# Kernel optimization log

Hardware: AMD Instinct MI355X
Metric: run time of the kernel (lower is better)

Reference implementation:

```python
import jax, jax.numpy as jnp
import numpy as np

N = 50000     # nodes
E = 600000    # directed edges (avg degree 12)
F_IN = 128    # num_features
H = 128       # hidden_units
C = 16        # num_classes
G = 500       # graphs in batch


def setup_inputs() -> dict:
    key = jax.random.key(0)
    ks = jax.random.split(key, 6)
    x = jax.random.normal(ks[0], (N, F_IN), jnp.float32)
    edge_src = jax.random.randint(ks[1], (E,), 0, N, jnp.int32)
    edge_dst = jax.random.randint(ks[2], (E,), 0, N, jnp.int32)
    batch = jnp.sort(jax.random.randint(ks[3], (N,), 0, G, jnp.int32))
    W1 = jax.random.normal(ks[4], (F_IN, H), jnp.float32) / np.float32(np.sqrt(F_IN))
    b1 = jnp.zeros((H,), jnp.float32)
    W2 = jax.random.normal(ks[5], (H, C), jnp.float32) / np.float32(np.sqrt(H))
    b2 = jnp.zeros((C,), jnp.float32)
    return {"x": x, "W1": W1, "b1": b1, "W2": W2, "b2": b2,
            "edge_src": edge_src, "edge_dst": edge_dst, "batch": batch}


def _gcn_conv(x, W, b, src, dst, norm):
    # linear transform then normalized scatter-add aggregation (PyG GCNConv)
    h = x @ W                                   # [N, out]
    msg = h[src] * norm[:, None]                # [E+N, out]
    return jax.ops.segment_sum(msg, dst, num_segments=N) + b


def reference(x, W1, b1, W2, b2, edge_src, edge_dst, batch):
    # add self-loops
    loops = jnp.arange(N, dtype=edge_src.dtype)
    src = jnp.concatenate([edge_src, loops])
    dst = jnp.concatenate([edge_dst, loops])
    # symmetric normalization D^-1/2 A D^-1/2 (in-degree at targets)
    deg = jax.ops.segment_sum(jnp.ones_like(dst, jnp.float32), dst, num_segments=N)
    dis = jax.lax.rsqrt(deg)  # deg >= 1 because of self-loops
    norm = dis[src] * dis[dst]

    h = jax.nn.relu(_gcn_conv(x, W1, b1, src, dst, norm))
    h = _gcn_conv(h, W2, b2, src, dst, norm)

    # scatter_mean pooling over graphs
    counts = jax.ops.segment_sum(jnp.ones((N,), jnp.float32), batch, num_segments=G)
    pooled = jax.ops.segment_sum(h, batch, num_segments=G) / jnp.maximum(counts, 1.0)[:, None]
    return jax.nn.log_softmax(pooled, axis=1)
```

## Files before the change

kernel.cpp:

```cpp
#include <hip/hip_runtime.h>
#include <hip/hip_bf16.h>


#define NN 50000
#define EE 600000
#define FIN 128
#define HH 128
#define CC 16
#define GG 500
#define ETOT (EE + NN)
#define SBLK 196

typedef unsigned short ushort_t;
typedef unsigned int uint_t;

typedef __attribute__((ext_vector_type(8))) short bf16x8;
typedef __attribute__((ext_vector_type(8))) ushort_t u16x8;
typedef __attribute__((ext_vector_type(4))) ushort_t u16x4;
typedef __attribute__((ext_vector_type(4))) float f32x4;
typedef __attribute__((ext_vector_type(2))) float f32x2;

__device__ inline ushort_t f2bf(float f) {
    uint_t u = __float_as_uint(f);
    u = (u + 0x7FFFu + ((u >> 16) & 1u)) >> 16;
    return (ushort_t)u;
}
__device__ inline float bf2f(ushort_t b) {
    return __uint_as_float(((uint_t)b) << 16);
}

__global__ void init_kernel(int* cnt, float* pooled) {
    int i = blockIdx.x * blockDim.x + threadIdx.x;
    if (i < NN) cnt[i] = 0;
    if (i < GG * CC) pooled[i] = 0.0f;
}

__global__ void count_kernel(const int* __restrict__ edge_dst,
                             int* __restrict__ cnt, int* __restrict__ seq) {
    int idx = blockIdx.x * blockDim.x + threadIdx.x;
    if (idx < EE) seq[idx] = atomicAdd(&cnt[edge_dst[idx]], 1);
}

__device__ inline int block_excl_scan(int v, int t, int* total) {
    __shared__ int wsum[4];
    int lane = t & 63, wv = t >> 6;
    int inc = v;
    for (int off = 1; off < 64; off <<= 1) {
        int n = __shfl_up(inc, off);
        if (lane >= off) inc += n;
    }
    if (lane == 63) wsum[wv] = inc;
    __syncthreads();
    int off_w = 0;
    for (int w = 0; w < wv; w++) off_w += wsum[w];
    *total = wsum[0] + wsum[1] + wsum[2] + wsum[3];
    return off_w + inc - v;
}

__global__ __launch_bounds__(256) void scanA_kernel(const int* __restrict__ cnt,
                                                    int* __restrict__ rowptr,
                                                    float* __restrict__ dis,
                                                    int* __restrict__ bsum) {
    int t = threadIdx.x;
    int i = blockIdx.x * 256 + t;
    int d = 0;
    if (i < NN) {
        d = cnt[i] + 1;
        dis[i] = rsqrtf((float)d);
    }
    int total;
    int excl = block_excl_scan(d, t, &total);
    if (i < NN) rowptr[i] = excl;
    if (t == 0) bsum[blockIdx.x] = total;
}

__global__ __launch_bounds__(256) void scanBC_kernel(int* __restrict__ rowptr,
                                                     const int* __restrict__ bsum) {
    __shared__ int sb[256];
    int t = threadIdx.x;
    int v = (t < SBLK) ? bsum[t] : 0;
    int total;
    int ex = block_excl_scan(v, t, &total);
    sb[t] = ex;
    __syncthreads();
    int myoff = sb[blockIdx.x];
    int i = blockIdx.x * 256 + t;
    if (i < NN) rowptr[i] += myoff;
    if (blockIdx.x == 0 && t == 0) rowptr[NN] = ETOT;
}

__global__ void fill_kernel(const int* __restrict__ edge_src,
                            const int* __restrict__ edge_dst,
                            const int* __restrict__ rowptr,
                            const int* __restrict__ seq,
                            int* __restrict__ csr) {
    int idx = blockIdx.x * blockDim.x + threadIdx.x;
    if (idx < EE) {
        int d = edge_dst[idx];
        csr[rowptr[d] + seq[idx]] = edge_src[idx];
    } else if (idx < ETOT) {
        int n = idx - EE;
        csr[rowptr[n + 1] - 1] = n;
    }
}

__global__ __launch_bounds__(256) void gemm1_kernel(const float* __restrict__ x,
                                                    const float* __restrict__ W1,
                                                    const float* __restrict__ dis,
                                                    unsigned char* __restrict__ hb8) {
    __shared__ ushort_t xs[64 * 136];
    __shared__ ushort_t wt[128 * 136];
    int t = threadIdx.x;
    int row0 = blockIdx.x * 64;
    for (int i = 0; i < 8; i++) {
        int slot = t + i * 256;
        int r = slot >> 5, k4 = slot & 31;
        int gr = row0 + r;
        float4 v = (gr < NN) ? ((const float4*)x)[gr * 32 + k4]
                             : make_float4(0.f, 0.f, 0.f, 0.f);
        u16x4 bv = { f2bf(v.x), f2bf(v.y), f2bf(v.z), f2bf(v.w) };
        *(u16x4*)(&xs[r * 136 + k4 * 4]) = bv;
    }
    for (int i = 0; i < 16; i++) {
        int slot = t + i * 256;
        int k = slot >> 5, c4 = slot & 31;
        float4 v = ((const float4*)W1)[k * 32 + c4];
        wt[(c4 * 4 + 0) * 136 + k] = f2bf(v.x);
        wt[(c4 * 4 + 1) * 136 + k] = f2bf(v.y);
        wt[(c4 * 4 + 2) * 136 + k] = f2bf(v.z);
        wt[(c4 * 4 + 3) * 136 + k] = f2bf(v.w);
    }
    __syncthreads();

    int wave = t >> 6, lane = t & 63;
    int m = lane & 15, quad = lane >> 4;
    f32x4 acc[8];
    for (int ct = 0; ct < 8; ct++) acc[ct] = (f32x4)(0.0f);

    for (int ko = 0; ko < 4; ko++) {
        bf16x8 a = *(const bf16x8*)(&xs[(16 * wave + m) * 136 + ko * 32 + quad * 8]);
        for (int ct = 0; ct < 8; ct++) {
            bf16x8 b = *(const bf16x8*)(&wt[(ct * 16 + m) * 136 + ko * 32 + quad * 8]);
            acc[ct] = __builtin_amdgcn_mfma_f32_16x16x32_bf16(a, b, acc[ct], 0, 0, 0);
        }
    }
    float dsc[4];
    for (int r = 0; r < 4; r++) {
        int grow = row0 + wave * 16 + quad * 4 + r;
        dsc[r] = (grow < NN) ? dis[grow] : 0.0f;
    }
    for (int ct = 0; ct < 8; ct++) {
        int gcol = ct * 16 + m;
        for (int r = 0; r < 4; r++) {
            int grow = row0 + wave * 16 + quad * 4 + r;
            if (grow < NN) {
                int p = __builtin_amdgcn_cvt_pk_fp8_f32(acc[ct][r] * dsc[r], 0.0f, 0, false);
                hb8[(size_t)grow * HH + gcol] = (unsigned char)(p & 0xFF);
            }
        }
    }
}

__global__ __launch_bounds__(256) void agg1_kernel(const unsigned char* __restrict__ hb8,
                                                   const int* __restrict__ rowptr,
                                                   const int* __restrict__ csr,
                                                   const float* __restrict__ dis,
                                                   const float* __restrict__ b1,
                                                   ushort_t* __restrict__ h1b) {
    int wave = threadIdx.x >> 6, lane = threadIdx.x & 63;
    int node = blockIdx.x * 4 + wave;
    if (node >= NN) return;
    int slot = lane >> 3, sub = lane & 7;
    int e0 = rowptr[node], e1 = rowptr[node + 1];
    float acc[16];
    for (int j = 0; j < 16; j++) acc[j] = 0.0f;
    for (int e = e0 + slot; e < e1; e += 8) {
        int s = csr[e];
        uint4 hv = *(const uint4*)(hb8 + (size_t)s * HH + sub * 16);
        uint_t words[4] = { hv.x, hv.y, hv.z, hv.w };
        for (int q = 0; q < 4; q++) {
            f32x2 lo = __builtin_amdgcn_cvt_pk_f32_fp8(words[q], false);
            f32x2 hi = __builtin_amdgcn_cvt_pk_f32_fp8(words[q], true);
            acc[q * 4 + 0] += lo[0];
            acc[q * 4 + 1] += lo[1];
            acc[q * 4 + 2] += hi[0];
            acc[q * 4 + 3] += hi[1];
        }
    }
    for (int j = 0; j < 16; j++) {
        acc[j] += __shfl_xor(acc[j], 8);
        acc[j] += __shfl_xor(acc[j], 16);
        acc[j] += __shfl_xor(acc[j], 32);
    }
    if (slot == 0) {
        float dn = dis[node];
        u16x8 o0, o1;
        for (int j = 0; j < 8; j++) {
            o0[j] = f2bf(fmaxf(acc[j]     * dn + b1[sub * 16 + j],     0.0f));
            o1[j] = f2bf(fmaxf(acc[8 + j] * dn + b1[sub * 16 + 8 + j], 0.0f));
        }
        *(u16x8*)(h1b + (size_t)node * HH + sub * 16)     = o0;
        *(u16x8*)(h1b + (size_t)node * HH + sub * 16 + 8) = o1;
    }
}

__global__ __launch_bounds__(256) void gemm2_kernel(const ushort_t* __restrict__ h1b,
                                                    const float* __restrict__ W2,
                                                    const float* __restrict__ dis,
                                                    ushort_t* __restrict__ h2b) {
    __shared__ ushort_t w2s[HH * CC];
    int t = threadIdx.x;
    for (int i = t; i < HH * CC; i += 256) w2s[i] = f2bf(W2[i]);
    __syncthreads();
    int wave = t >> 6, lane = t & 63;
    int m = lane & 15, quad = lane >> 4;
    int node0 = (blockIdx.x * 4 + wave) * 16;
    f32x4 acc = (f32x4)(0.0f);
    int arow = node0 + m;
    for (int ko = 0; ko < 4; ko++) {
        bf16x8 a = (bf16x8)(short)0;
        if (arow < NN)
            a = *(const bf16x8*)(h1b + (size_t)arow * HH + ko * 32 + quad * 8);
        bf16x8 b;
        for (int j = 0; j < 8; j++)
            b[j] = (short)w2s[(ko * 32 + quad * 8 + j) * CC + m];
        acc = __builtin_amdgcn_mfma_f32_16x16x32_bf16(a, b, acc, 0, 0, 0);
    }
    for (int r = 0; r < 4; r++) {
        int grow = node0 + quad * 4 + r;
        if (grow < NN) h2b[grow * CC + m] = f2bf(acc[r] * dis[grow]);
    }
}

__global__ __launch_bounds__(256) void agg2pool_kernel(const ushort_t* __restrict__ h2b,
                                                       const int* __restrict__ rowptr,
                                                       const int* __restrict__ csr,
                                                       const float* __restrict__ dis,
                                                       const float* __restrict__ b2,
                                                       const int* __restrict__ batch,
                                                       float* __restrict__ pooled) {
    __shared__ float vals[16][16];
    __shared__ int gid[16];
    int t = threadIdx.x;
    int local = t >> 4, c = t & 15;
    int node = blockIdx.x * 16 + local;
    int e0 = rowptr[node], e1 = rowptr[node + 1];
    float acc = 0.0f;
    for (int e = e0; e < e1; e++) {
        acc += bf2f(h2b[(size_t)csr[e] * CC + c]);
    }
    vals[local][c] = acc * dis[node] + b2[c];
    if (c == 0) gid[local] = batch[node];
    __syncthreads();
    if (t < 16) {
        float run = 0.0f;
        for (int i = 0; i < 16; i++) {
            run += vals[i][t];
            if (i == 15 || gid[i + 1] != gid[i]) {
                atomicAdd(&pooled[gid[i] * CC + t], run);
                run = 0.0f;
            }
        }
    }
}

__global__ void lsm_kernel(const float* __restrict__ pooled,
                           const int* __restrict__ batch,
                           float* __restrict__ out) {
    int idx = blockIdx.x * blockDim.x + threadIdx.x;
    int g = idx >> 4, c = idx & 15;
    if (g >= GG) return;
    int lo = 0, hi = NN;
    while (lo < hi) { int mid = (lo + hi) >> 1; if (batch[mid] < g) lo = mid + 1; else hi = mid; }
    int lo2 = lo, hi2 = NN;
    while (lo2 < hi2) { int mid = (lo2 + hi2) >> 1; if (batch[mid] < g + 1) lo2 = mid + 1; else hi2 = mid; }
    float cnt = (float)(lo2 - lo);
    float v = pooled[g * CC + c] / fmaxf(cnt, 1.0f);
    float m = v;
    for (int off = 8; off >= 1; off >>= 1) m = fmaxf(m, __shfl_xor(m, off, 16));
    float s = expf(v - m);
    for (int off = 8; off >= 1; off >>= 1) s += __shfl_xor(s, off, 16);
    out[g * CC + c] = v - m - logf(s);
}

extern "C" void kernel_launch(void* const* d_in, const int* in_sizes, int n_in,
                              void* d_out, int out_size, void* d_ws, size_t ws_size,
                              hipStream_t stream) {
    const float* x  = (const float*)d_in[0];
    const float* W1 = (const float*)d_in[1];
    const float* b1 = (const float*)d_in[2];
    const float* W2 = (const float*)d_in[3];
    const float* b2 = (const float*)d_in[4];
    const int* edge_src = (const int*)d_in[5];
    const int* edge_dst = (const int*)d_in[6];
    const int* batch    = (const int*)d_in[7];
    float* out = (float*)d_out;

    char* ws = (char*)d_ws;
    size_t off = 0;
    auto alloc = [&](size_t bytes) {
        void* p = ws + off;
        off += (bytes + 255) & ~size_t(255);
        return p;
    };
    int*   cnt     = (int*)  alloc(NN * 4);
    float* dis     = (float*)alloc(NN * 4);
    int*   rowptr  = (int*)  alloc((NN + 1) * 4);
    int*   seq     = (int*)  alloc(EE * 4);
    int*   bsum    = (int*)  alloc(SBLK * 4);
    int*   csr     = (int*)  alloc((size_t)ETOT * 4);
    unsigned char* hb8 = (unsigned char*)alloc((size_t)NN * HH);
    ushort_t* h1b  = (ushort_t*)alloc((size_t)NN * HH * 2);
    ushort_t* h2b  = (ushort_t*)alloc((size_t)NN * CC * 2);
    float* pooled  = (float*)alloc(GG * CC * 4);

    const int B = 256;
    init_kernel<<<(NN + B - 1) / B, B, 0, stream>>>(cnt, pooled);
    count_kernel<<<(EE + B - 1) / B, B, 0, stream>>>(edge_dst, cnt, seq);
    scanA_kernel<<<SBLK, B, 0, stream>>>(cnt, rowptr, dis, bsum);
    scanBC_kernel<<<SBLK, B, 0, stream>>>(rowptr, bsum);
    fill_kernel<<<(ETOT + B - 1) / B, B, 0, stream>>>(edge_src, edge_dst, rowptr, seq, csr);
    gemm1_kernel<<<(NN + 63) / 64, B, 0, stream>>>(x, W1, dis, hb8);
    agg1_kernel<<<(NN + 3) / 4, B, 0, stream>>>(hb8, rowptr, csr, dis, b1, h1b);
    gemm2_kernel<<<(NN + 63) / 64, B, 0, stream>>>(h1b, W2, dis, h2b);
    agg2pool_kernel<<<NN / 16, B, 0, stream>>>(h2b, rowptr, csr, dis, b2, batch, pooled);
    lsm_kernel<<<(GG * CC + B - 1) / B, B, 0, stream>>>(pooled, batch, out);
}
```

Measured before the change: 211.4 us.

## Fuse GEMM1 with edge counting, fuse GEMM2 into aggregation, pack norms into CSR

GEMM1 now runs in the same launch as the degree-counting atomics, with one block in four doing matmul work, so it no longer waits on the degree scan. Because of that, the source-side normalisation moves out of GEMM1 and is stored as an fp16 weight packed into each CSR entry next to a 16-bit source index. The second linear layer (128x16) is fused into the first aggregation kernel with FP32 FMAs, which drops the bf16 h1 buffer and the separate gemm2 launch. In exchange, each gathered edge now costs an extra multiply, and the 16-bit index field cannot represent node ids of 65536 or more (this graph has 50,000 nodes).

```diff
diff --git a/kernel.cpp b/kernel.cpp
--- a/kernel.cpp
+++ b/kernel.cpp
@@ -10,12 +10,13 @@
 #define GG 500
 #define ETOT (EE + NN)
 #define SBLK 196
+#define GB 782
+#define PB 3126
 
 typedef unsigned short ushort_t;
 typedef unsigned int uint_t;
 
 typedef __attribute__((ext_vector_type(8))) short bf16x8;
-typedef __attribute__((ext_vector_type(8))) ushort_t u16x8;
 typedef __attribute__((ext_vector_type(4))) ushort_t u16x4;
 typedef __attribute__((ext_vector_type(4))) float f32x4;
 typedef __attribute__((ext_vector_type(2))) float f32x2;
@@ -28,6 +29,12 @@
 __device__ inline float bf2f(ushort_t b) {
     return __uint_as_float(((uint_t)b) << 16);
 }
+__device__ inline ushort_t f2h(float f) {
+    _Float16 h = (_Float16)f; ushort_t u; __builtin_memcpy(&u, &h, 2); return u;
+}
+__device__ inline float h2f(ushort_t u) {
+    _Float16 h; __builtin_memcpy(&h, &u, 2); return (float)h;
+}
 
 __global__ void init_kernel(int* cnt, float* pooled) {
     int i = blockIdx.x * blockDim.x + threadIdx.x;
@@ -35,10 +42,64 @@
     if (i < GG * CC) pooled[i] = 0.0f;
 }
 
-__global__ void count_kernel(const int* __restrict__ edge_dst,
-                             int* __restrict__ cnt, int* __restrict__ seq) {
-    int idx = blockIdx.x * blockDim.x + threadIdx.x;
-    if (idx < EE) seq[idx] = atomicAdd(&cnt[edge_dst[idx]], 1);
+__global__ __launch_bounds__(256) void phase1_kernel(const int* __restrict__ edge_dst,
+                                                     int* __restrict__ cnt,
+                                                     int* __restrict__ seq,
+                                                     const float* __restrict__ x,
+                                                     const float* __restrict__ W1,
+                                                     unsigned char* __restrict__ hb8) {
+    __shared__ ushort_t xs[64 * 136];
+    __shared__ ushort_t wt[128 * 136];
+    int bid = blockIdx.x;
+    int t = threadIdx.x;
+    if ((bid & 3) == 0) {
+        int row0 = (bid >> 2) * 64;
+        for (int i = 0; i < 8; i++) {
+            int slot = t + i * 256;
+            int r = slot >> 5, k4 = slot & 31;
+            int gr = row0 + r;
+            float4 v = (gr < NN) ? ((const float4*)x)[gr * 32 + k4]
+                                 : make_float4(0.f, 0.f, 0.f, 0.f);
+            u16x4 bv = { f2bf(v.x), f2bf(v.y), f2bf(v.z), f2bf(v.w) };
+            *(u16x4*)(&xs[r * 136 + k4 * 4]) = bv;
+        }
+        for (int i = 0; i < 16; i++) {
+            int slot = t + i * 256;
+            int k = slot >> 5, c4 = slot & 31;
+            float4 v = ((const float4*)W1)[k * 32 + c4];
+            wt[(c4 * 4 + 0) * 136 + k] = f2bf(v.x);
+            wt[(c4 * 4 + 1) * 136 + k] = f2bf(v.y);
+            wt[(c4 * 4 + 2) * 136 + k] = f2bf(v.z);
+            wt[(c4 * 4 + 3) * 136 + k] = f2bf(v.w);
+        }
+        __syncthreads();
+
+        int wave = t >> 6, lane = t & 63;
+        int m = lane & 15, quad = lane >> 4;
+        f32x4 acc[8];
+        for (int ct = 0; ct < 8; ct++) acc[ct] = (f32x4)(0.0f);
+        for (int ko = 0; ko < 4; ko++) {
+            bf16x8 a = *(const bf16x8*)(&xs[(16 * wave + m) * 136 + ko * 32 + quad * 8]);
+            for (int ct = 0; ct < 8; ct++) {
+                bf16x8 b = *(const bf16x8*)(&wt[(ct * 16 + m) * 136 + ko * 32 + quad * 8]);
+                acc[ct] = __builtin_amdgcn_mfma_f32_16x16x32_bf16(a, b, acc[ct], 0, 0, 0);
+            }
+        }
+        for (int ct = 0; ct < 8; ct++) {
+            int gcol = ct * 16 + m;
+            for (int r = 0; r < 4; r++) {
+                int grow = row0 + wave * 16 + quad * 4 + r;
+                if (grow < NN) {
+                    int p = __builtin_amdgcn_cvt_pk_fp8_f32(acc[ct][r], 0.0f, 0, false);
+                    hb8[(size_t)grow * HH + gcol] = (unsigned char)(p & 0xFF);
+                }
+            }
+        }
+    } else {
+        int cidx = bid - (bid >> 2) - 1;
+        int idx = cidx * 256 + t;
+        if (idx < EE) seq[idx] = atomicAdd(&cnt[edge_dst[idx]], 1);
+    }
 }
 
 __device__ inline int block_excl_scan(int v, int t, int* total) {
@@ -91,150 +152,81 @@
 
 __global__ void fill_kernel(const int* __restrict__ edge_src,
                             const int* __restrict__ edge_dst,
+                            const float* __restrict__ dis,
                             const int* __restrict__ rowptr,
                             const int* __restrict__ seq,
-                            int* __restrict__ csr) {
+                            uint_t* __restrict__ csr) {
     int idx = blockIdx.x * blockDim.x + threadIdx.x;
     if (idx < EE) {
-        int d = edge_dst[idx];
-        csr[rowptr[d] + seq[idx]] = edge_src[idx];
+        int s = edge_src[idx], d = edge_dst[idx];
+        csr[rowptr[d] + seq[idx]] = (uint_t)s | ((uint_t)f2h(dis[s]) << 16);
     } else if (idx < ETOT) {
         int n = idx - EE;
-        csr[rowptr[n + 1] - 1] = n;
-    }
-}
-
-__global__ __launch_bounds__(256) void gemm1_kernel(const float* __restrict__ x,
-                                                    const float* __restrict__ W1,
-                                                    const float* __restrict__ dis,
-                                                    unsigned char* __restrict__ hb8) {
-    __shared__ ushort_t xs[64 * 136];
-    __shared__ ushort_t wt[128 * 136];
-    int t = threadIdx.x;
-    int row0 = blockIdx.x * 64;
-    for (int i = 0; i < 8; i++) {
-        int slot = t + i * 256;
-        int r = slot >> 5, k4 = slot & 31;
-        int gr = row0 + r;
-        float4 v = (gr < NN) ? ((const float4*)x)[gr * 32 + k4]
-                             : make_float4(0.f, 0.f, 0.f, 0.f);
-        u16x4 bv = { f2bf(v.x), f2bf(v.y), f2bf(v.z), f2bf(v.w) };
-        *(u16x4*)(&xs[r * 136 + k4 * 4]) = bv;
-    }
-    for (int i = 0; i < 16; i++) {
-        int slot = t + i * 256;
-        int k = slot >> 5, c4 = slot & 31;
-        float4 v = ((const float4*)W1)[k * 32 + c4];
-        wt[(c4 * 4 + 0) * 136 + k] = f2bf(v.x);
-        wt[(c4 * 4 + 1) * 136 + k] = f2bf(v.y);
-        wt[(c4 * 4 + 2) * 136 + k] = f2bf(v.z);
-        wt[(c4 * 4 + 3) * 136 + k] = f2bf(v.w);
-    }
-    __syncthreads();
-
-    int wave = t >> 6, lane = t & 63;
-    int m = lane & 15, quad = lane >> 4;
-    f32x4 acc[8];
-    for (int ct = 0; ct < 8; ct++) acc[ct] = (f32x4)(0.0f);
-
-    for (int ko = 0; ko < 4; ko++) {
-        bf16x8 a = *(const bf16x8*)(&xs[(16 * wave + m) * 136 + ko * 32 + quad * 8]);
-        for (int ct = 0; ct < 8; ct++) {
-            bf16x8 b = *(const bf16x8*)(&wt[(ct * 16 + m) * 136 + ko * 32 + quad * 8]);
-            acc[ct] = __builtin_amdgcn_mfma_f32_16x16x32_bf16(a, b, acc[ct], 0, 0, 0);
-        }
-    }
-    float dsc[4];
-    for (int r = 0; r < 4; r++) {
-        int grow = row0 + wave * 16 + quad * 4 + r;
-        dsc[r] = (grow < NN) ? dis[grow] : 0.0f;
-    }
-    for (int ct = 0; ct < 8; ct++) {
-        int gcol = ct * 16 + m;
-        for (int r = 0; r < 4; r++) {
-            int grow = row0 + wave * 16 + quad * 4 + r;
-            if (grow < NN) {
-                int p = __builtin_amdgcn_cvt_pk_fp8_f32(acc[ct][r] * dsc[r], 0.0f, 0, false);
-                hb8[(size_t)grow * HH + gcol] = (unsigned char)(p & 0xFF);
-            }
-        }
+        csr[rowptr[n + 1] - 1] = (uint_t)n | ((uint_t)f2h(dis[n]) << 16);
     }
 }
 
 __global__ __launch_bounds__(256) void agg1_kernel(const unsigned char* __restrict__ hb8,
                                                    const int* __restrict__ rowptr,
-                                                   const int* __restrict__ csr,
+                                                   const uint_t* __restrict__ csr,
                                                    const float* __restrict__ dis,
                                                    const float* __restrict__ b1,
-                                                   ushort_t* __restrict__ h1b) {
-    int wave = threadIdx.x >> 6, lane = threadIdx.x & 63;
-    int node = blockIdx.x * 4 + wave;
-    if (node >= NN) return;
-    int slot = lane >> 3, sub = lane & 7;
-    int e0 = rowptr[node], e1 = rowptr[node + 1];
-    float acc[16];
-    for (int j = 0; j < 16; j++) acc[j] = 0.0f;
-    for (int e = e0 + slot; e < e1; e += 8) {
-        int s = csr[e];
-        uint4 hv = *(const uint4*)(hb8 + (size_t)s * HH + sub * 16);
-        uint_t words[4] = { hv.x, hv.y, hv.z, hv.w };
-        for (int q = 0; q < 4; q++) {
-            f32x2 lo = __builtin_amdgcn_cvt_pk_f32_fp8(words[q], false);
-            f32x2 hi = __builtin_amdgcn_cvt_pk_f32_fp8(words[q], true);
-            acc[q * 4 + 0] += lo[0];
-            acc[q * 4 + 1] += lo[1];
-            acc[q * 4 + 2] += hi[0];
-            acc[q * 4 + 3] += hi[1];
-        }
-    }
-    for (int j = 0; j < 16; j++) {
-        acc[j] += __shfl_xor(acc[j], 8);
-        acc[j] += __shfl_xor(acc[j], 16);
-        acc[j] += __shfl_xor(acc[j], 32);
-    }
-    if (slot == 0) {
-        float dn = dis[node];
-        u16x8 o0, o1;
-        for (int j = 0; j < 8; j++) {
-            o0[j] = f2bf(fmaxf(acc[j]     * dn + b1[sub * 16 + j],     0.0f));
-            o1[j] = f2bf(fmaxf(acc[8 + j] * dn + b1[sub * 16 + 8 + j], 0.0f));
-        }
-        *(u16x8*)(h1b + (size_t)node * HH + sub * 16)     = o0;
-        *(u16x8*)(h1b + (size_t)node * HH + sub * 16 + 8) = o1;
-    }
-}
-
-__global__ __launch_bounds__(256) void gemm2_kernel(const ushort_t* __restrict__ h1b,
-                                                    const float* __restrict__ W2,
-                                                    const float* __restrict__ dis,
-                                                    ushort_t* __restrict__ h2b) {
-    __shared__ ushort_t w2s[HH * CC];
-    int t = threadIdx.x;
-    for (int i = t; i < HH * CC; i += 256) w2s[i] = f2bf(W2[i]);
+                                                   const float* __restrict__ W2,
+                                                   ushort_t* __restrict__ h2b) {
+    __shared__ float w2s[HH * CC];
+    __shared__ float b1s[HH];
+    int t = threadIdx.x;
+    for (int i = t; i < HH * CC; i += 256) w2s[i] = W2[i];
+    if (t < HH) b1s[t] = b1[t];
     __syncthreads();
     int wave = t >> 6, lane = t & 63;
-    int m = lane & 15, quad = lane >> 4;
-    int node0 = (blockIdx.x * 4 + wave) * 16;
-    f32x4 acc = (f32x4)(0.0f);
-    int arow = node0 + m;
-    for (int ko = 0; ko < 4; ko++) {
-        bf16x8 a = (bf16x8)(short)0;
-        if (arow < NN)
-            a = *(const bf16x8*)(h1b + (size_t)arow * HH + ko * 32 + quad * 8);
-        bf16x8 b;
-        for (int j = 0; j < 8; j++)
-            b[j] = (short)w2s[(ko * 32 + quad * 8 + j) * CC + m];
-        acc = __builtin_amdgcn_mfma_f32_16x16x32_bf16(a, b, acc, 0, 0, 0);
-    }
-    for (int r = 0; r < 4; r++) {
-        int grow = node0 + quad * 4 + r;
-        if (grow < NN) h2b[grow * CC + m] = f2bf(acc[r] * dis[grow]);
+    int slot = lane >> 3, sub = lane & 7;
+    for (int it = 0; it < 4; it++) {
+        int node = blockIdx.x * 16 + wave * 4 + it;
+        int e0 = rowptr[node], e1 = rowptr[node + 1];
+        float acc[16];
+        for (int j = 0; j < 16; j++) acc[j] = 0.0f;
+        for (int e = e0 + slot; e < e1; e += 8) {
+            uint_t ent = csr[e];
+            float w = h2f((ushort_t)(ent >> 16));
+            uint4 hv = *(const uint4*)(hb8 + (size_t)(ent & 0xFFFFu) * HH + sub * 16);
+            uint_t words[4] = { hv.x, hv.y, hv.z, hv.w };
+            for (int q = 0; q < 4; q++) {
+                f32x2 lo = __builtin_amdgcn_cvt_pk_f32_fp8(words[q], false);
+                f32x2 hi = __builtin_amdgcn_cvt_pk_f32_fp8(words[q], true);
+                acc[q * 4 + 0] += w * lo[0];
+                acc[q * 4 + 1] += w * lo[1];
+                acc[q * 4 + 2] += w * hi[0];
+                acc[q * 4 + 3] += w * hi[1];
+            }
+        }
+        for (int j = 0; j < 16; j++) {
+            acc[j] += __shfl_xor(acc[j], 8);
+            acc[j] += __shfl_xor(acc[j], 16);
+            acc[j] += __shfl_xor(acc[j], 32);
+        }
+        float dn = dis[node];
+        float h1v[16];
+        for (int j = 0; j < 16; j++)
+            h1v[j] = fmaxf(dn * acc[j] + b1s[sub * 16 + j], 0.0f);
+        float p0 = 0.0f, p1 = 0.0f;
+        for (int j = 0; j < 16; j++) {
+            float hv = h1v[j];
+            p0 += hv * w2s[(sub * 16 + j) * CC + 2 * slot];
+            p1 += hv * w2s[(sub * 16 + j) * CC + 2 * slot + 1];
+        }
+        p0 += __shfl_xor(p0, 1); p0 += __shfl_xor(p0, 2); p0 += __shfl_xor(p0, 4);
+        p1 += __shfl_xor(p1, 1); p1 += __shfl_xor(p1, 2); p1 += __shfl_xor(p1, 4);
+        if (sub == 0) {
+            uint_t packed = (uint_t)f2bf(p0) | ((uint_t)f2bf(p1) << 16);
+            *(uint_t*)(h2b + (size_t)node * CC + 2 * slot) = packed;
+        }
     }
 }
 
 __global__ __launch_bounds__(256) void agg2pool_kernel(const ushort_t* __restrict__ h2b,
                                                        const int* __restrict__ rowptr,
-                                                       const int* __restrict__ csr,
+                                                       const uint_t* __restrict__ csr,
                                                        const float* __restrict__ dis,
                                                        const float* __restrict__ b2,
                                                        const int* __restrict__ batch,
@@ -247,7 +239,8 @@
     int e0 = rowptr[node], e1 = rowptr[node + 1];
     float acc = 0.0f;
     for (int e = e0; e < e1; e++) {
-        acc += bf2f(h2b[(size_t)csr[e] * CC + c]);
+        uint_t ent = csr[e];
+        acc += h2f((ushort_t)(ent >> 16)) * bf2f(h2b[(size_t)(ent & 0xFFFFu) * CC + c]);
     }
     vals[local][c] = acc * dis[node] + b2[c];
     if (c == 0) gid[local] = batch[node];
@@ -308,21 +301,19 @@
     int*   rowptr  = (int*)  alloc((NN + 1) * 4);
     int*   seq     = (int*)  alloc(EE * 4);
     int*   bsum    = (int*)  alloc(SBLK * 4);
-    int*   csr     = (int*)  alloc((size_t)ETOT * 4);
+    uint_t* csr    = (uint_t*)alloc((size_t)ETOT * 4);
     unsigned char* hb8 = (unsigned char*)alloc((size_t)NN * HH);
-    ushort_t* h1b  = (ushort_t*)alloc((size_t)NN * HH * 2);
     ushort_t* h2b  = (ushort_t*)alloc((size_t)NN * CC * 2);
     float* pooled  = (float*)alloc(GG * CC * 4);
 
     const int B = 256;
     init_kernel<<<(NN + B - 1) / B, B, 0, stream>>>(cnt, pooled);
-    count_kernel<<<(EE + B - 1) / B, B, 0, stream>>>(edge_dst, cnt, seq);
+    phase1_kernel<<<PB, B, 0, stream>>>(edge_dst, cnt, seq, x, W1, hb8);
     scanA_kernel<<<SBLK, B, 0, stream>>>(cnt, rowptr, dis, bsum);
     scanBC_kernel<<<SBLK, B, 0, stream>>>(rowptr, bsum);
-    fill_kernel<<<(ETOT + B - 1) / B, B, 0, stream>>>(edge_src, edge_dst, rowptr, seq, csr);
-    gemm1_kernel<<<(NN + 63) / 64, B, 0, stream>>>(x, W1, dis, hb8);
-    agg1_kernel<<<(NN + 3) / 4, B, 0, stream>>>(hb8, rowptr, csr, dis, b1, h1b);
-    gemm2_kernel<<<(NN + 63) / 64, B, 0, stream>>>(h1b, W2, dis, h2b);
+    fill_kernel<<<(ETOT + B - 1) / B, B, 0, stream>>>(edge_src, edge_dst, dis,
+                                                      rowptr, seq, csr);
+    agg1_kernel<<<NN / 16, B, 0, stream>>>(hb8, rowptr, csr, dis, b1, W2, h2b);
     agg2pool_kernel<<<NN / 16, B, 0, stream>>>(h2b, rowptr, csr, dis, b2, batch, pooled);
     lsm_kernel<<<(GG * CC + B - 1) / B, B, 0, stream>>>(pooled, batch, out);
 }
```

New measurement: 243.4 us. 1.15x slower.
